# Performance work log

Hardware: AMD Instinct MI355X
Metric: run time of the kernel (lower is better)

The kernel has to match this reference:

```python
import jax, jax.numpy as jnp
import numpy as np

EPS = 1e-5  # torch nn.LayerNorm default eps


def layer_norm(x, w, b):
    mu = jnp.mean(x, axis=-1, keepdims=True)
    var = jnp.mean(jnp.square(x - mu), axis=-1, keepdims=True)
    return (x - mu) * jax.lax.rsqrt(var + EPS) * w + b


def setup_inputs() -> dict:
    key = jax.random.key(0)
    k1, k2 = jax.random.split(key)
    B, T, D, N = 8, 1024, 512, 8192
    x = jax.random.normal(k1, (B, T, D), dtype=jnp.float32)
    ln_weight = jnp.ones((D,), dtype=jnp.float32)
    ln_bias = jnp.zeros((D,), dtype=jnp.float32)
    embd = jax.random.normal(k2, (N, D), dtype=jnp.float32)
    return {"x": x, "ln_weight": ln_weight, "ln_bias": ln_bias, "embd": embd}


def reference(x, ln_weight, ln_bias, embd):
    # LayerNorm
    h = layer_norm(x, ln_weight, ln_bias)            # [B, T, D]
    # codebook logits + argmax select
    logits = jnp.einsum("btd,nd->btn", h, embd)      # [B, T, N]
    idxs = jnp.argmax(logits, axis=-1)               # [B, T]
    q1 = embd[idxs]                                  # [B, T, D] gather
    # straight-through combine
    q2 = h + jax.lax.stop_gradient(q1 - h)
    quantize = (q1 + q2) / 2
    return quantize, idxs
```

## Files before the change

### kernel.cpp

```cpp
#include <hip/hip_runtime.h>
#include <hip/hip_bf16.h>

#define ROWS   8192
#define DIM    512
#define NCODES 8192
#define BM     256
#define BN     128
#define BK     64
#define NT     (DIM / BK)
#define MARGIN 3.0f

using i32x4 = __attribute__((ext_vector_type(4))) int;
typedef unsigned char u8;

__device__ __forceinline__ void gload_lds16(const void* g, void* l) {
    __builtin_amdgcn_global_load_lds((const __attribute__((address_space(1))) void*)g,
                                     (__attribute__((address_space(3))) void*)l,
                                     16, 0, 0);
}

__device__ __forceinline__ unsigned int pack4(int a, int b, int c, int d) {
    return (a & 255) | ((b & 255) << 8) | ((c & 255) << 16) | ((unsigned)(d & 255) << 24);
}

__global__ __launch_bounds__(256) void prep_kernel(
    const float* __restrict__ x, const float* __restrict__ lw,
    const float* __restrict__ lb, const float* __restrict__ embd,
    float2* __restrict__ stats, float* __restrict__ sh, float* __restrict__ se,
    u8* __restrict__ Hq, u8* __restrict__ Eq)
{
    __shared__ float red[4];
    const int w    = threadIdx.x >> 6;
    const int lane = threadIdx.x & 63;
    const int b    = blockIdx.x;

    if (b < 2048) {
        const int row = b * 4 + w;
        const float* xr = x + (size_t)row * DIM + lane * 8;
        float4 v0 = *(const float4*)(xr);
        float4 v1 = *(const float4*)(xr + 4);
        float s = (v0.x + v0.y) + (v0.z + v0.w) + (v1.x + v1.y) + (v1.z + v1.w);
        float q = v0.x*v0.x + v0.y*v0.y + v0.z*v0.z + v0.w*v0.w
                + v1.x*v1.x + v1.y*v1.y + v1.z*v1.z + v1.w*v1.w;
        #pragma unroll
        for (int off = 1; off < 64; off <<= 1) {
            s += __shfl_xor(s, off);
            q += __shfl_xor(q, off);
        }
        float mu   = s * (1.0f / DIM);
        float var  = q * (1.0f / DIM) - mu * mu;
        float rstd = rsqrtf(var + 1e-5f);
        if (lane == 0) stats[row] = make_float2(mu, rstd);

        float4 w0 = *(const float4*)(lw + lane * 8);
        float4 w1 = *(const float4*)(lw + lane * 8 + 4);
        float4 b0 = *(const float4*)(lb + lane * 8);
        float4 b1 = *(const float4*)(lb + lane * 8 + 4);
        float hv[8] = {
            (v0.x - mu) * rstd * w0.x + b0.x, (v0.y - mu) * rstd * w0.y + b0.y,
            (v0.z - mu) * rstd * w0.z + b0.z, (v0.w - mu) * rstd * w0.w + b0.w,
            (v1.x - mu) * rstd * w1.x + b1.x, (v1.y - mu) * rstd * w1.y + b1.y,
            (v1.z - mu) * rstd * w1.z + b1.z, (v1.w - mu) * rstd * w1.w + b1.w };

        float am = 0.0f;
        #pragma unroll
        for (int j = 0; j < 8; ++j) am = fmaxf(am, fabsf(hv[j]));
        #pragma unroll
        for (int off = 1; off < 64; off <<= 1) am = fmaxf(am, __shfl_xor(am, off));
        const float inv = (am > 0.0f) ? (127.0f / am) : 0.0f;
        if (lane == 0) sh[row] = am * (1.0f / 127.0f);

        int qi[8];
        #pragma unroll
        for (int j = 0; j < 8; ++j) qi[j] = __float2int_rn(hv[j] * inv);
        uint2 p = make_uint2(pack4(qi[0], qi[1], qi[2], qi[3]),
                             pack4(qi[4], qi[5], qi[6], qi[7]));
        *(uint2*)(Hq + (size_t)row * DIM + lane * 8) = p;
    } else {
        const int chunk = b - 2048;
        const int row   = chunk * 64 + (threadIdx.x >> 2);
        const int off0  = (threadIdx.x & 3) * 128;
        const float* er = embd + (size_t)row * DIM + off0;

        float4 v[32];
        float am = 0.0f;
        #pragma unroll
        for (int j = 0; j < 32; ++j) {
            v[j] = *(const float4*)(er + j * 4);
            am = fmaxf(am, fmaxf(fmaxf(fabsf(v[j].x), fabsf(v[j].y)),
                                 fmaxf(fabsf(v[j].z), fabsf(v[j].w))));
        }
        #pragma unroll
        for (int off = 1; off < 64; off <<= 1) am = fmaxf(am, __shfl_xor(am, off));
        if (lane == 0) red[w] = am;
        __syncthreads();
        am = fmaxf(fmaxf(red[0], red[1]), fmaxf(red[2], red[3]));

        const float inv = (am > 0.0f) ? (127.0f / am) : 0.0f;
        if (threadIdx.x == 0) se[chunk] = am * (1.0f / 127.0f);

        u8* out = Eq + (size_t)row * DIM + off0;
        #pragma unroll
        for (int j = 0; j < 32; j += 4) {
            uint4 o;
            o.x = pack4(__float2int_rn(v[j+0].x*inv), __float2int_rn(v[j+0].y*inv),
                        __float2int_rn(v[j+0].z*inv), __float2int_rn(v[j+0].w*inv));
            o.y = pack4(__float2int_rn(v[j+1].x*inv), __float2int_rn(v[j+1].y*inv),
                        __float2int_rn(v[j+1].z*inv), __float2int_rn(v[j+1].w*inv));
            o.z = pack4(__float2int_rn(v[j+2].x*inv), __float2int_rn(v[j+2].y*inv),
                        __float2int_rn(v[j+2].z*inv), __float2int_rn(v[j+2].w*inv));
            o.w = pack4(__float2int_rn(v[j+3].x*inv), __float2int_rn(v[j+3].y*inv),
                        __float2int_rn(v[j+3].z*inv), __float2int_rn(v[j+3].w*inv));
            *(uint4*)(out + j * 4) = o;
        }
    }
}

__global__ __launch_bounds__(256, 2) void gemm_argmax_kernel(
    const u8* __restrict__ Hq, const u8* __restrict__ Eq,
    const float* __restrict__ sh, const float* __restrict__ se,
    float* __restrict__ pval, int* __restrict__ pidx)
{
    __shared__ __align__(16) u8 As[3][BM * BK];
    __shared__ __align__(16) u8 Bs[3][BN * BK];

    const int tid  = threadIdx.x;
    const int w    = tid >> 6;
    const int lane = tid & 63;
    const int r_   = lane & 15;
    const int g    = lane >> 4;
    const int wr   = w >> 1;
    const int wc   = w & 1;

    const int bid  = blockIdx.x;
    const int trow = ((bid & 7) << 2) | ((bid >> 3) & 3);
    const int tcol = bid >> 5;
    const int r0 = trow * BM;
    const int n0 = tcol * BN;

    const int da0 = (w * 4 + 0) * 16 + (lane >> 2);
    const int da1 = (w * 4 + 1) * 16 + (lane >> 2);
    const int da2 = (w * 4 + 2) * 16 + (lane >> 2);
    const int da3 = (w * 4 + 3) * 16 + (lane >> 2);
    const int db0 = (w * 2 + 0) * 16 + (lane >> 2);
    const int db1 = (w * 2 + 1) * 16 + (lane >> 2);
    const int lc  = (lane & 3) * 16;
    const u8* sA0 = Hq + (size_t)(r0 + da0) * DIM + (lc ^ (((da0 >> 1) & 3) << 4));
    const u8* sA1 = Hq + (size_t)(r0 + da1) * DIM + (lc ^ (((da1 >> 1) & 3) << 4));
    const u8* sA2 = Hq + (size_t)(r0 + da2) * DIM + (lc ^ (((da2 >> 1) & 3) << 4));
    const u8* sA3 = Hq + (size_t)(r0 + da3) * DIM + (lc ^ (((da3 >> 1) & 3) << 4));
    const u8* sB0 = Eq + (size_t)(n0 + db0) * DIM + (lc ^ (((db0 >> 1) & 3) << 4));
    const u8* sB1 = Eq + (size_t)(n0 + db1) * DIM + (lc ^ (((db1 >> 1) & 3) << 4));
    const int ua0 = (w * 4 + 0) * 1024, ua1 = (w * 4 + 1) * 1024;
    const int ua2 = (w * 4 + 2) * 1024, ua3 = (w * 4 + 3) * 1024;
    const int ub0 = (w * 2 + 0) * 1024, ub1 = (w * 2 + 1) * 1024;

    const int swz   = ((r_ >> 1) & 3) << 4;
    const int abase = (wr * 128 + r_) * 64 + ((g * 16) ^ swz);
    const int bbase = (wc * 64  + r_) * 64 + ((g * 16) ^ swz);

    i32x4 acc[8][4];
    #pragma unroll
    for (int m = 0; m < 8; ++m)
        #pragma unroll
        for (int n = 0; n < 4; ++n) acc[m][n] = (i32x4){0, 0, 0, 0};

#define STAGE(T, SL) do {                                           \
        const int _ko = (T) * BK;                                   \
        gload_lds16(sA0 + _ko, &As[SL][ua0]);                       \
        gload_lds16(sA1 + _ko, &As[SL][ua1]);                       \
        gload_lds16(sA2 + _ko, &As[SL][ua2]);                       \
        gload_lds16(sA3 + _ko, &As[SL][ua3]);                       \
        gload_lds16(sB0 + _ko, &Bs[SL][ub0]);                       \
        gload_lds16(sB1 + _ko, &Bs[SL][ub1]);                       \
    } while (0)
#define MF(M, N, AV, BV) \
        acc[M][N] = __builtin_amdgcn_mfma_i32_16x16x64_i8(AV, BV, acc[M][N], 0, 0, 0)

#define K_TILE(SL, STG, VMSTR) do {                                 \
        STG;                                                        \
        asm volatile("s_waitcnt vmcnt(" VMSTR ")" ::: "memory");    \
        __builtin_amdgcn_s_barrier();                               \
        const char* Ab = (const char*)&As[SL][0];                   \
        const char* Bb = (const char*)&Bs[SL][0];                   \
        i32x4 a0 = *(const i32x4*)(Ab + abase + 0 * 1024);          \
        i32x4 a1 = *(const i32x4*)(Ab + abase + 1 * 1024);          \
        i32x4 a2 = *(const i32x4*)(Ab + abase + 2 * 1024);          \
        i32x4 a3 = *(const i32x4*)(Ab + abase + 3 * 1024);          \
        i32x4 a4 = *(const i32x4*)(Ab + abase + 4 * 1024);          \
        i32x4 a5 = *(const i32x4*)(Ab + abase + 5 * 1024);          \
        i32x4 a6 = *(const i32x4*)(Ab + abase + 6 * 1024);          \
        i32x4 a7 = *(const i32x4*)(Ab + abase + 7 * 1024);          \
        i32x4 b0 = *(const i32x4*)(Bb + bbase + 0 * 1024);          \
        i32x4 b1 = *(const i32x4*)(Bb + bbase + 1 * 1024);          \
        i32x4 b2 = *(const i32x4*)(Bb + bbase + 2 * 1024);          \
        i32x4 b3 = *(const i32x4*)(Bb + bbase + 3 * 1024);          \
        __builtin_amdgcn_s_setprio(1);                              \
        MF(0, 0, a0, b0); MF(0, 1, a0, b1); MF(0, 2, a0, b2); MF(0, 3, a0, b3); \
        MF(1, 0, a1, b0); MF(1, 1, a1, b1); MF(1, 2, a1, b2); MF(1, 3, a1, b3); \
        MF(2, 0, a2, b0); MF(2, 1, a2, b1); MF(2, 2, a2, b2); MF(2, 3, a2, b3); \
        MF(3, 0, a3, b0); MF(3, 1, a3, b1); MF(3, 2, a3, b2); MF(3, 3, a3, b3); \
        MF(4, 0, a4, b0); MF(4, 1, a4, b1); MF(4, 2, a4, b2); MF(4, 3, a4, b3); \
        MF(5, 0, a5, b0); MF(5, 1, a5, b1); MF(5, 2, a5, b2); MF(5, 3, a5, b3); \
        MF(6, 0, a6, b0); MF(6, 1, a6, b1); MF(6, 2, a6, b2); MF(6, 3, a6, b3); \
        MF(7, 0, a7, b0); MF(7, 1, a7, b1); MF(7, 2, a7, b2); MF(7, 3, a7, b3); \
        __builtin_amdgcn_s_setprio(0);                              \
        __builtin_amdgcn_s_barrier();                               \
    } while (0)

    STAGE(0, 0);
    STAGE(1, 1);

    K_TILE(0, STAGE(2, 2), "12");
    K_TILE(1, STAGE(3, 0), "12");
    K_TILE(2, STAGE(4, 1), "12");
    K_TILE(0, STAGE(5, 2), "12");
    K_TILE(1, STAGE(6, 0), "12");
    K_TILE(2, STAGE(7, 1), "12");
    K_TILE(0, , "6");
    K_TILE(1, , "0");

#undef K_TILE
#undef MF
#undef STAGE

    const int cb    = n0 + wc * 64;
    const float se_ch = se[tcol * 2 + wc];
    #pragma unroll
    for (int m = 0; m < 8; ++m) {
        const float4 sc4 = *(const float4*)&sh[r0 + wr * 128 + m * 16 + g * 4];
        #pragma unroll
        for (int reg = 0; reg < 4; ++reg) {
            int ka = (acc[m][0][reg] << 7) | (63 - r_);
            int kb = (acc[m][1][reg] << 7) | (47 - r_);
            int kc = (acc[m][2][reg] << 7) | (31 - r_);
            int kd = (acc[m][3][reg] << 7) | (15 - r_);
            int m1 = max(ka, kb), n1 = min(ka, kb);
            int m2 = max(kc, kd), n2 = min(kc, kd);
            int k1 = max(m1, m2);
            int k2 = max(min(m1, m2), max(n1, n2));
            #pragma unroll
            for (int off = 1; off < 16; off <<= 1) {
                int b1 = __shfl_xor(k1, off);
                int b2 = __shfl_xor(k2, off);
                k2 = max(max(k2, b2), min(k1, b1));
                k1 = max(k1, b1);
            }
            if (r_ == 0) {
                const float sc = (reg == 0) ? sc4.x : (reg == 1) ? sc4.y
                                 : (reg == 2) ? sc4.z : sc4.w;
                const int row = r0 + wr * 128 + m * 16 + g * 4 + reg;
                const size_t base = (size_t)row * 256 + (tcol * 2 + wc) * 2;
                pval[base]     = (float)(k1 >> 7) * (sc * se_ch);
                pval[base + 1] = (float)(k2 >> 7) * (sc * se_ch);
                pidx[base]     = cb + 63 - (k1 & 63);
                pidx[base + 1] = cb + 63 - (k2 & 63);
            }
        }
    }
}

__global__ __launch_bounds__(256) void finalize_kernel(
    const float* __restrict__ x, const float* __restrict__ lw,
    const float* __restrict__ lb, const float* __restrict__ embd,
    const float2* __restrict__ stats,
    const float* __restrict__ pval, const int* __restrict__ pidx,
    float* __restrict__ outq, float* __restrict__ outi)
{
    const int w    = threadIdx.x >> 6;
    const int lane = threadIdx.x & 63;
    const int row  = blockIdx.x * 4 + w;

    const float4 cv = *(const float4*)&pval[(size_t)row * 256 + lane * 4];
    const int4   ci = *(const int4*)  &pidx[(size_t)row * 256 + lane * 4];
    float vv[4] = { cv.x, cv.y, cv.z, cv.w };
    int   ii[4] = { ci.x, ci.y, ci.z, ci.w };

    float M = fmaxf(fmaxf(vv[0], vv[1]), fmaxf(vv[2], vv[3]));
    #pragma unroll
    for (int off = 1; off < 64; off <<= 1) M = fmaxf(M, __shfl_xor(M, off));
    const float T = M - MARGIN;

    const float2 st = stats[row];
    const float mu = st.x, rstd = st.y;
    const float* xr = x + (size_t)row * DIM + lane * 8;
    float4 x0 = *(const float4*)(xr);
    float4 x1 = *(const float4*)(xr + 4);
    float4 w0 = *(const float4*)(lw + lane * 8);
    float4 w1 = *(const float4*)(lw + lane * 8 + 4);
    float4 b0 = *(const float4*)(lb + lane * 8);
    float4 b1 = *(const float4*)(lb + lane * 8 + 4);
    float h[8] = {
        (x0.x - mu) * rstd * w0.x + b0.x, (x0.y - mu) * rstd * w0.y + b0.y,
        (x0.z - mu) * rstd * w0.z + b0.z, (x0.w - mu) * rstd * w0.w + b0.w,
        (x1.x - mu) * rstd * w1.x + b1.x, (x1.y - mu) * rstd * w1.y + b1.y,
        (x1.z - mu) * rstd * w1.z + b1.z, (x1.w - mu) * rstd * w1.w + b1.w };

    float bestv = -3.4e38f; int besti = 0x7fffffff;
    #pragma unroll
    for (int s = 0; s < 4; ++s) {
        unsigned long long msk = __ballot(vv[s] >= T);
        while (msk) {
            const int L = __ffsll(msk) - 1;
            msk &= msk - 1;
            const int cand = __shfl(ii[s], L);
            const float* er = embd + (size_t)cand * DIM + lane * 8;
            float4 e0 = *(const float4*)er;
            float4 e1 = *(const float4*)(er + 4);
            float d = h[0]*e0.x + h[1]*e0.y + h[2]*e0.z + h[3]*e0.w
                    + h[4]*e1.x + h[5]*e1.y + h[6]*e1.z + h[7]*e1.w;
            #pragma unroll
            for (int off = 1; off < 64; off <<= 1) d += __shfl_xor(d, off);
            if (d > bestv || (d == bestv && cand < besti)) { bestv = d; besti = cand; }
        }
    }

    const float* er = embd + (size_t)besti * DIM + lane * 8;
    float4 q0 = *(const float4*)er;
    float4 q1 = *(const float4*)(er + 4);
    float* qr = outq + (size_t)row * DIM + lane * 8;
    *(float4*)(qr)     = q0;
    *(float4*)(qr + 4) = q1;
    if (lane == 0) outi[row] = (float)besti;
}

extern "C" void kernel_launch(void* const* d_in, const int* in_sizes, int n_in,
                              void* d_out, int out_size, void* d_ws, size_t ws_size,
                              hipStream_t stream) {
    const float* x    = (const float*)d_in[0];
    const float* lnw  = (const float*)d_in[1];
    const float* lnb  = (const float*)d_in[2];
    const float* embd = (const float*)d_in[3];

    float* outq = (float*)d_out;
    float* outi = outq + (size_t)ROWS * DIM;

    char* ws = (char*)d_ws;
    float2* stats = (float2*)ws;
    float*  sh    = (float*)(ws + (1 << 16));
    float*  se    = (float*)(ws + (1 << 16) + (1 << 15));
    u8*     Hq    = (u8*)(ws + (1 << 17));
    u8*     Eq    = (u8*)(ws + (1 << 17) + (4 << 20));
    float*  pval  = (float*)(ws + (1 << 17) + (8 << 20));
    int*    pidx  = (int*)  (ws + (1 << 17) + (16 << 20));

    prep_kernel<<<2176, 256, 0, stream>>>(x, lnw, lnb, embd, stats, sh, se, Hq, Eq);

    gemm_argmax_kernel<<<2048, 256, 0, stream>>>(Hq, Eq, sh, se, pval, pidx);

    finalize_kernel<<<ROWS / 4, 256, 0, stream>>>(x, lnw, lnb, embd, stats,
                                                  pval, pidx, outq, outi);
}
```

Before: 107.8 us.

## Drop LDS staging; load MFMA fragments directly from global per wave

Replaces the 4-wave block, which staged A/B tiles through triple-buffered LDS with async global-to-LDS loads and barriers, with single-wave blocks. Each wave computes a 128x64 output tile and loads i8 MFMA fragments straight from global memory into registers, double-buffered across K steps. This removes LDS traffic and barriers, but drops cross-wave data sharing, so global/L2 traffic per output rises and loads are 16-byte strided accesses across rows.

```diff
diff --git a/kernel.cpp b/kernel.cpp
--- a/kernel.cpp
+++ b/kernel.cpp
@@ -4,20 +4,11 @@
 #define ROWS   8192
 #define DIM    512
 #define NCODES 8192
-#define BM     256
-#define BN     128
-#define BK     64
-#define NT     (DIM / BK)
+#define NT     8
 #define MARGIN 3.0f
 
 using i32x4 = __attribute__((ext_vector_type(4))) int;
 typedef unsigned char u8;
-
-__device__ __forceinline__ void gload_lds16(const void* g, void* l) {
-    __builtin_amdgcn_global_load_lds((const __attribute__((address_space(1))) void*)g,
-                                     (__attribute__((address_space(3))) void*)l,
-                                     16, 0, 0);
-}
 
 __device__ __forceinline__ unsigned int pack4(int a, int b, int c, int d) {
     return (a & 255) | ((b & 255) << 8) | ((c & 255) << 16) | ((unsigned)(d & 255) << 24);
@@ -116,48 +107,23 @@
     }
 }
 
-__global__ __launch_bounds__(256, 2) void gemm_argmax_kernel(
+__global__ __launch_bounds__(64, 2) void gemm_argmax_kernel(
     const u8* __restrict__ Hq, const u8* __restrict__ Eq,
     const float* __restrict__ sh, const float* __restrict__ se,
     float* __restrict__ pval, int* __restrict__ pidx)
 {
-    __shared__ __align__(16) u8 As[3][BM * BK];
-    __shared__ __align__(16) u8 Bs[3][BN * BK];
-
-    const int tid  = threadIdx.x;
-    const int w    = tid >> 6;
-    const int lane = tid & 63;
+    const int lane = threadIdx.x;
     const int r_   = lane & 15;
     const int g    = lane >> 4;
-    const int wr   = w >> 1;
-    const int wc   = w & 1;
 
     const int bid  = blockIdx.x;
-    const int trow = ((bid & 7) << 2) | ((bid >> 3) & 3);
-    const int tcol = bid >> 5;
-    const int r0 = trow * BM;
-    const int n0 = tcol * BN;
-
-    const int da0 = (w * 4 + 0) * 16 + (lane >> 2);
-    const int da1 = (w * 4 + 1) * 16 + (lane >> 2);
-    const int da2 = (w * 4 + 2) * 16 + (lane >> 2);
-    const int da3 = (w * 4 + 3) * 16 + (lane >> 2);
-    const int db0 = (w * 2 + 0) * 16 + (lane >> 2);
-    const int db1 = (w * 2 + 1) * 16 + (lane >> 2);
-    const int lc  = (lane & 3) * 16;
-    const u8* sA0 = Hq + (size_t)(r0 + da0) * DIM + (lc ^ (((da0 >> 1) & 3) << 4));
-    const u8* sA1 = Hq + (size_t)(r0 + da1) * DIM + (lc ^ (((da1 >> 1) & 3) << 4));
-    const u8* sA2 = Hq + (size_t)(r0 + da2) * DIM + (lc ^ (((da2 >> 1) & 3) << 4));
-    const u8* sA3 = Hq + (size_t)(r0 + da3) * DIM + (lc ^ (((da3 >> 1) & 3) << 4));
-    const u8* sB0 = Eq + (size_t)(n0 + db0) * DIM + (lc ^ (((db0 >> 1) & 3) << 4));
-    const u8* sB1 = Eq + (size_t)(n0 + db1) * DIM + (lc ^ (((db1 >> 1) & 3) << 4));
-    const int ua0 = (w * 4 + 0) * 1024, ua1 = (w * 4 + 1) * 1024;
-    const int ua2 = (w * 4 + 2) * 1024, ua3 = (w * 4 + 3) * 1024;
-    const int ub0 = (w * 2 + 0) * 1024, ub1 = (w * 2 + 1) * 1024;
-
-    const int swz   = ((r_ >> 1) & 3) << 4;
-    const int abase = (wr * 128 + r_) * 64 + ((g * 16) ^ swz);
-    const int bbase = (wc * 64  + r_) * 64 + ((g * 16) ^ swz);
+    const int rowp = ((bid & 7) << 3) | ((bid >> 3) & 7);
+    const int colp = bid >> 6;
+    const int r0   = rowp * 128;
+    const int n0   = colp * 64;
+
+    const u8* Ab = Hq + (size_t)(r0 + r_) * DIM + g * 16;
+    const u8* Bb = Eq + (size_t)(n0 + r_) * DIM + g * 16;
 
     i32x4 acc[8][4];
     #pragma unroll
@@ -165,70 +131,43 @@
         #pragma unroll
         for (int n = 0; n < 4; ++n) acc[m][n] = (i32x4){0, 0, 0, 0};
 
-#define STAGE(T, SL) do {                                           \
-        const int _ko = (T) * BK;                                   \
-        gload_lds16(sA0 + _ko, &As[SL][ua0]);                       \
-        gload_lds16(sA1 + _ko, &As[SL][ua1]);                       \
-        gload_lds16(sA2 + _ko, &As[SL][ua2]);                       \
-        gload_lds16(sA3 + _ko, &As[SL][ua3]);                       \
-        gload_lds16(sB0 + _ko, &Bs[SL][ub0]);                       \
-        gload_lds16(sB1 + _ko, &Bs[SL][ub1]);                       \
+    i32x4 af[2][8], bf[2][4];
+
+#define LOADT(P, KT) do {                                              \
+        _Pragma("unroll")                                              \
+        for (int m = 0; m < 8; ++m)                                    \
+            af[P][m] = *(const i32x4*)(Ab + (size_t)m * 16 * DIM + (KT) * 64); \
+        _Pragma("unroll")                                              \
+        for (int n = 0; n < 4; ++n)                                    \
+            bf[P][n] = *(const i32x4*)(Bb + (size_t)n * 16 * DIM + (KT) * 64); \
     } while (0)
 #define MF(M, N, AV, BV) \
         acc[M][N] = __builtin_amdgcn_mfma_i32_16x16x64_i8(AV, BV, acc[M][N], 0, 0, 0)
 
-#define K_TILE(SL, STG, VMSTR) do {                                 \
-        STG;                                                        \
-        asm volatile("s_waitcnt vmcnt(" VMSTR ")" ::: "memory");    \
-        __builtin_amdgcn_s_barrier();                               \
-        const char* Ab = (const char*)&As[SL][0];                   \
-        const char* Bb = (const char*)&Bs[SL][0];                   \
-        i32x4 a0 = *(const i32x4*)(Ab + abase + 0 * 1024);          \
-        i32x4 a1 = *(const i32x4*)(Ab + abase + 1 * 1024);          \
-        i32x4 a2 = *(const i32x4*)(Ab + abase + 2 * 1024);          \
-        i32x4 a3 = *(const i32x4*)(Ab + abase + 3 * 1024);          \
-        i32x4 a4 = *(const i32x4*)(Ab + abase + 4 * 1024);          \
-        i32x4 a5 = *(const i32x4*)(Ab + abase + 5 * 1024);          \
-        i32x4 a6 = *(const i32x4*)(Ab + abase + 6 * 1024);          \
-        i32x4 a7 = *(const i32x4*)(Ab + abase + 7 * 1024);          \
-        i32x4 b0 = *(const i32x4*)(Bb + bbase + 0 * 1024);          \
-        i32x4 b1 = *(const i32x4*)(Bb + bbase + 1 * 1024);          \
-        i32x4 b2 = *(const i32x4*)(Bb + bbase + 2 * 1024);          \
-        i32x4 b3 = *(const i32x4*)(Bb + bbase + 3 * 1024);          \
-        __builtin_amdgcn_s_setprio(1);                              \
-        MF(0, 0, a0, b0); MF(0, 1, a0, b1); MF(0, 2, a0, b2); MF(0, 3, a0, b3); \
-        MF(1, 0, a1, b0); MF(1, 1, a1, b1); MF(1, 2, a1, b2); MF(1, 3, a1, b3); \
-        MF(2, 0, a2, b0); MF(2, 1, a2, b1); MF(2, 2, a2, b2); MF(2, 3, a2, b3); \
-        MF(3, 0, a3, b0); MF(3, 1, a3, b1); MF(3, 2, a3, b2); MF(3, 3, a3, b3); \
-        MF(4, 0, a4, b0); MF(4, 1, a4, b1); MF(4, 2, a4, b2); MF(4, 3, a4, b3); \
-        MF(5, 0, a5, b0); MF(5, 1, a5, b1); MF(5, 2, a5, b2); MF(5, 3, a5, b3); \
-        MF(6, 0, a6, b0); MF(6, 1, a6, b1); MF(6, 2, a6, b2); MF(6, 3, a6, b3); \
-        MF(7, 0, a7, b0); MF(7, 1, a7, b1); MF(7, 2, a7, b2); MF(7, 3, a7, b3); \
-        __builtin_amdgcn_s_setprio(0);                              \
-        __builtin_amdgcn_s_barrier();                               \
-    } while (0)
-
-    STAGE(0, 0);
-    STAGE(1, 1);
-
-    K_TILE(0, STAGE(2, 2), "12");
-    K_TILE(1, STAGE(3, 0), "12");
-    K_TILE(2, STAGE(4, 1), "12");
-    K_TILE(0, STAGE(5, 2), "12");
-    K_TILE(1, STAGE(6, 0), "12");
-    K_TILE(2, STAGE(7, 1), "12");
-    K_TILE(0, , "6");
-    K_TILE(1, , "0");
-
-#undef K_TILE
+    LOADT(0, 0);
+    #pragma unroll
+    for (int t = 0; t < NT; ++t) {
+        const int cur = t & 1;
+        if (t + 1 < NT) LOADT(cur ^ 1, t + 1);
+        __builtin_amdgcn_s_setprio(1);
+        #pragma unroll
+        for (int m = 0; m < 8; ++m) {
+            MF(m, 0, af[cur][m], bf[cur][0]);
+            MF(m, 1, af[cur][m], bf[cur][1]);
+            MF(m, 2, af[cur][m], bf[cur][2]);
+            MF(m, 3, af[cur][m], bf[cur][3]);
+        }
+        __builtin_amdgcn_s_setprio(0);
+    }
+
 #undef MF
-#undef STAGE
-
-    const int cb    = n0 + wc * 64;
-    const float se_ch = se[tcol * 2 + wc];
+#undef LOADT
+
+    const int   cb    = n0;
+    const float se_ch = se[colp];
     #pragma unroll
     for (int m = 0; m < 8; ++m) {
-        const float4 sc4 = *(const float4*)&sh[r0 + wr * 128 + m * 16 + g * 4];
+        const float4 sc4 = *(const float4*)&sh[r0 + m * 16 + g * 4];
         #pragma unroll
         for (int reg = 0; reg < 4; ++reg) {
             int ka = (acc[m][0][reg] << 7) | (63 - r_);
@@ -249,8 +188,8 @@
             if (r_ == 0) {
                 const float sc = (reg == 0) ? sc4.x : (reg == 1) ? sc4.y
                                  : (reg == 2) ? sc4.z : sc4.w;
-                const int row = r0 + wr * 128 + m * 16 + g * 4 + reg;
-                const size_t base = (size_t)row * 256 + (tcol * 2 + wc) * 2;
+                const int row = r0 + m * 16 + g * 4 + reg;
+                const size_t base = (size_t)row * 256 + colp * 2;
                 pval[base]     = (float)(k1 >> 7) * (sc * se_ch);
                 pval[base + 1] = (float)(k2 >> 7) * (sc * se_ch);
                 pidx[base]     = cb + 63 - (k1 & 63);
@@ -346,7 +285,7 @@
 
     prep_kernel<<<2176, 256, 0, stream>>>(x, lnw, lnb, embd, stats, sh, se, Hq, Eq);
 
-    gemm_argmax_kernel<<<2048, 256, 0, stream>>>(Hq, Eq, sh, se, pval, pidx);
+    gemm_argmax_kernel<<<8192, 64, 0, stream>>>(Hq, Eq, sh, se, pval, pidx);
 
     finalize_kernel<<<ROWS / 4, 256, 0, stream>>>(x, lnw, lnb, embd, stats,
                                                   pval, pidx, outq, outi);
```

Result: slower. 152.7 us (+41.6%).

## Load A fragments directly from global to registers, ring-buffer B in LDS

Applied to the files above, without the earlier changes.

The quantized activation tile (A) no longer goes through LDS. Each wave now reads its MFMA A fragments straight from global memory into registers, one K-step ahead. B stays staged in LDS, now in a 4-slot ring, which lets the trailing per-tile barrier go. The aim is to cut LDS traffic, LDS footprint and one barrier per K-step. The cost is exposed global-load latency for A, since the prefetch lands only one tile ahead and the compiler must insert waits, plus redundant A reads across the two column waves.

```diff
diff --git a/kernel.cpp b/kernel.cpp
--- a/kernel.cpp
+++ b/kernel.cpp
@@ -121,8 +121,7 @@
     const float* __restrict__ sh, const float* __restrict__ se,
     float* __restrict__ pval, int* __restrict__ pidx)
 {
-    __shared__ __align__(16) u8 As[3][BM * BK];
-    __shared__ __align__(16) u8 Bs[3][BN * BK];
+    __shared__ __align__(16) u8 Bs[4][BN * BK];
 
     const int tid  = threadIdx.x;
     const int w    = tid >> 6;
@@ -138,26 +137,17 @@
     const int r0 = trow * BM;
     const int n0 = tcol * BN;
 
-    const int da0 = (w * 4 + 0) * 16 + (lane >> 2);
-    const int da1 = (w * 4 + 1) * 16 + (lane >> 2);
-    const int da2 = (w * 4 + 2) * 16 + (lane >> 2);
-    const int da3 = (w * 4 + 3) * 16 + (lane >> 2);
     const int db0 = (w * 2 + 0) * 16 + (lane >> 2);
     const int db1 = (w * 2 + 1) * 16 + (lane >> 2);
     const int lc  = (lane & 3) * 16;
-    const u8* sA0 = Hq + (size_t)(r0 + da0) * DIM + (lc ^ (((da0 >> 1) & 3) << 4));
-    const u8* sA1 = Hq + (size_t)(r0 + da1) * DIM + (lc ^ (((da1 >> 1) & 3) << 4));
-    const u8* sA2 = Hq + (size_t)(r0 + da2) * DIM + (lc ^ (((da2 >> 1) & 3) << 4));
-    const u8* sA3 = Hq + (size_t)(r0 + da3) * DIM + (lc ^ (((da3 >> 1) & 3) << 4));
     const u8* sB0 = Eq + (size_t)(n0 + db0) * DIM + (lc ^ (((db0 >> 1) & 3) << 4));
     const u8* sB1 = Eq + (size_t)(n0 + db1) * DIM + (lc ^ (((db1 >> 1) & 3) << 4));
-    const int ua0 = (w * 4 + 0) * 1024, ua1 = (w * 4 + 1) * 1024;
-    const int ua2 = (w * 4 + 2) * 1024, ua3 = (w * 4 + 3) * 1024;
     const int ub0 = (w * 2 + 0) * 1024, ub1 = (w * 2 + 1) * 1024;
 
     const int swz   = ((r_ >> 1) & 3) << 4;
-    const int abase = (wr * 128 + r_) * 64 + ((g * 16) ^ swz);
-    const int bbase = (wc * 64  + r_) * 64 + ((g * 16) ^ swz);
+    const int bbase = (wc * 64 + r_) * 64 + ((g * 16) ^ swz);
+
+    const u8* Ab = Hq + (size_t)(r0 + wr * 128 + r_) * DIM + g * 16;
 
     i32x4 acc[8][4];
     #pragma unroll
@@ -165,64 +155,66 @@
         #pragma unroll
         for (int n = 0; n < 4; ++n) acc[m][n] = (i32x4){0, 0, 0, 0};
 
-#define STAGE(T, SL) do {                                           \
+    i32x4 af[8];
+
+#define STAGE_B(T) do {                                             \
         const int _ko = (T) * BK;                                   \
-        gload_lds16(sA0 + _ko, &As[SL][ua0]);                       \
-        gload_lds16(sA1 + _ko, &As[SL][ua1]);                       \
-        gload_lds16(sA2 + _ko, &As[SL][ua2]);                       \
-        gload_lds16(sA3 + _ko, &As[SL][ua3]);                       \
-        gload_lds16(sB0 + _ko, &Bs[SL][ub0]);                       \
-        gload_lds16(sB1 + _ko, &Bs[SL][ub1]);                       \
+        gload_lds16(sB0 + _ko, &Bs[(T) & 3][ub0]);                  \
+        gload_lds16(sB1 + _ko, &Bs[(T) & 3][ub1]);                  \
+    } while (0)
+#define LOAD_A(KT) do {                                             \
+        const int _ko = (KT) * BK;                                  \
+        af[0] = *(const i32x4*)(Ab + 0 * 8192 + _ko);               \
+        af[1] = *(const i32x4*)(Ab + 1 * 8192 + _ko);               \
+        af[2] = *(const i32x4*)(Ab + 2 * 8192 + _ko);               \
+        af[3] = *(const i32x4*)(Ab + 3 * 8192 + _ko);               \
+        af[4] = *(const i32x4*)(Ab + 4 * 8192 + _ko);               \
+        af[5] = *(const i32x4*)(Ab + 5 * 8192 + _ko);               \
+        af[6] = *(const i32x4*)(Ab + 6 * 8192 + _ko);               \
+        af[7] = *(const i32x4*)(Ab + 7 * 8192 + _ko);               \
     } while (0)
 #define MF(M, N, AV, BV) \
         acc[M][N] = __builtin_amdgcn_mfma_i32_16x16x64_i8(AV, BV, acc[M][N], 0, 0, 0)
 
-#define K_TILE(SL, STG, VMSTR) do {                                 \
-        STG;                                                        \
+#define K_TILE(T, VMSTR, DOSTG, DOA) do {                           \
+        if (DOSTG) STAGE_B((T) + 2);                                \
         asm volatile("s_waitcnt vmcnt(" VMSTR ")" ::: "memory");    \
         __builtin_amdgcn_s_barrier();                               \
-        const char* Ab = (const char*)&As[SL][0];                   \
-        const char* Bb = (const char*)&Bs[SL][0];                   \
-        i32x4 a0 = *(const i32x4*)(Ab + abase + 0 * 1024);          \
-        i32x4 a1 = *(const i32x4*)(Ab + abase + 1 * 1024);          \
-        i32x4 a2 = *(const i32x4*)(Ab + abase + 2 * 1024);          \
-        i32x4 a3 = *(const i32x4*)(Ab + abase + 3 * 1024);          \
-        i32x4 a4 = *(const i32x4*)(Ab + abase + 4 * 1024);          \
-        i32x4 a5 = *(const i32x4*)(Ab + abase + 5 * 1024);          \
-        i32x4 a6 = *(const i32x4*)(Ab + abase + 6 * 1024);          \
-        i32x4 a7 = *(const i32x4*)(Ab + abase + 7 * 1024);          \
-        i32x4 b0 = *(const i32x4*)(Bb + bbase + 0 * 1024);          \
-        i32x4 b1 = *(const i32x4*)(Bb + bbase + 1 * 1024);          \
-        i32x4 b2 = *(const i32x4*)(Bb + bbase + 2 * 1024);          \
-        i32x4 b3 = *(const i32x4*)(Bb + bbase + 3 * 1024);          \
+        const u8* Bp = &Bs[(T) & 3][0];                             \
+        i32x4 b0 = *(const i32x4*)(Bp + bbase + 0 * 1024);          \
+        i32x4 b1 = *(const i32x4*)(Bp + bbase + 1 * 1024);          \
+        i32x4 b2 = *(const i32x4*)(Bp + bbase + 2 * 1024);          \
+        i32x4 b3 = *(const i32x4*)(Bp + bbase + 3 * 1024);          \
         __builtin_amdgcn_s_setprio(1);                              \
-        MF(0, 0, a0, b0); MF(0, 1, a0, b1); MF(0, 2, a0, b2); MF(0, 3, a0, b3); \
-        MF(1, 0, a1, b0); MF(1, 1, a1, b1); MF(1, 2, a1, b2); MF(1, 3, a1, b3); \
-        MF(2, 0, a2, b0); MF(2, 1, a2, b1); MF(2, 2, a2, b2); MF(2, 3, a2, b3); \
-        MF(3, 0, a3, b0); MF(3, 1, a3, b1); MF(3, 2, a3, b2); MF(3, 3, a3, b3); \
-        MF(4, 0, a4, b0); MF(4, 1, a4, b1); MF(4, 2, a4, b2); MF(4, 3, a4, b3); \
-        MF(5, 0, a5, b0); MF(5, 1, a5, b1); MF(5, 2, a5, b2); MF(5, 3, a5, b3); \
-        MF(6, 0, a6, b0); MF(6, 1, a6, b1); MF(6, 2, a6, b2); MF(6, 3, a6, b3); \
-        MF(7, 0, a7, b0); MF(7, 1, a7, b1); MF(7, 2, a7, b2); MF(7, 3, a7, b3); \
+        MF(0, 0, af[0], b0); MF(0, 1, af[0], b1); MF(0, 2, af[0], b2); MF(0, 3, af[0], b3); \
+        MF(1, 0, af[1], b0); MF(1, 1, af[1], b1); MF(1, 2, af[1], b2); MF(1, 3, af[1], b3); \
+        MF(2, 0, af[2], b0); MF(2, 1, af[2], b1); MF(2, 2, af[2], b2); MF(2, 3, af[2], b3); \
+        MF(3, 0, af[3], b0); MF(3, 1, af[3], b1); MF(3, 2, af[3], b2); MF(3, 3, af[3], b3); \
+        MF(4, 0, af[4], b0); MF(4, 1, af[4], b1); MF(4, 2, af[4], b2); MF(4, 3, af[4], b3); \
+        MF(5, 0, af[5], b0); MF(5, 1, af[5], b1); MF(5, 2, af[5], b2); MF(5, 3, af[5], b3); \
+        MF(6, 0, af[6], b0); MF(6, 1, af[6], b1); MF(6, 2, af[6], b2); MF(6, 3, af[6], b3); \
+        MF(7, 0, af[7], b0); MF(7, 1, af[7], b1); MF(7, 2, af[7], b2); MF(7, 3, af[7], b3); \
         __builtin_amdgcn_s_setprio(0);                              \
-        __builtin_amdgcn_s_barrier();                               \
+        if (DOA) LOAD_A((T) + 1);                                   \
     } while (0)
 
-    STAGE(0, 0);
-    STAGE(1, 1);
-
-    K_TILE(0, STAGE(2, 2), "12");
-    K_TILE(1, STAGE(3, 0), "12");
-    K_TILE(2, STAGE(4, 1), "12");
-    K_TILE(0, STAGE(5, 2), "12");
-    K_TILE(1, STAGE(6, 0), "12");
-    K_TILE(2, STAGE(7, 1), "12");
-    K_TILE(0, , "6");
-    K_TILE(1, , "0");
+    STAGE_B(0);
+    STAGE_B(1);
+    LOAD_A(0);
+
+    K_TILE(0, "12", 1, 1);
+    K_TILE(1, "12", 1, 1);
+    K_TILE(2, "12", 1, 1);
+    K_TILE(3, "12", 1, 1);
+    K_TILE(4, "12", 1, 1);
+    K_TILE(5, "12", 1, 1);
+    K_TILE(6, "10", 0, 1);
+    K_TILE(7, "8",  0, 0);
 
 #undef K_TILE
 #undef MF
-#undef STAGE
+#undef LOAD_A
+#undef STAGE_B
 
     const int cb    = n0 + wc * 64;
     const float se_ch = se[tcol * 2 + wc];
```

Result: slower. 133.6 us (+23.9%).
